# Optimization experiments

Measured on AMD Instinct MI355X. Metric: run time of the kernel, lower is better.

The kernel has to match this reference:

```python
import jax, jax.numpy as jnp
import numpy as np

N = 50000
E = 800000
IN_C = 128
HID_C = 64
OUT_C = 64
HEADS = 4
NEG_SLOPE = 0.2


def setup_inputs() -> dict:
    key = jax.random.key(0)
    ks = jax.random.split(key, 12)
    x = jax.random.normal(ks[0], (N, IN_C), dtype=jnp.float32)
    edge_index = jax.random.randint(ks[1], (2, E), 0, N, dtype=jnp.int32)
    s = 0.1
    # layer 1 params (GATConv: shared lin for src/dst, att vectors per head, bias over H*C)
    W1 = jax.random.normal(ks[2], (IN_C, HEADS * HID_C), dtype=jnp.float32) * s
    att_src1 = jax.random.normal(ks[3], (HEADS, HID_C), dtype=jnp.float32) * s
    att_dst1 = jax.random.normal(ks[4], (HEADS, HID_C), dtype=jnp.float32) * s
    b1 = jnp.zeros((HEADS * HID_C,), dtype=jnp.float32)
    # layer 2 params
    W2 = jax.random.normal(ks[5], (HEADS * HID_C, HEADS * OUT_C), dtype=jnp.float32) * s
    att_src2 = jax.random.normal(ks[6], (HEADS, OUT_C), dtype=jnp.float32) * s
    att_dst2 = jax.random.normal(ks[7], (HEADS, OUT_C), dtype=jnp.float32) * s
    b2 = jnp.zeros((HEADS * OUT_C,), dtype=jnp.float32)
    return {"x": x, "edge_index": edge_index,
            "W1": W1, "att_src1": att_src1, "att_dst1": att_dst1, "b1": b1,
            "W2": W2, "att_src2": att_src2, "att_dst2": att_dst2, "b2": b2}


def _segment_softmax(e, dst, n):
    # e: [E, H], softmax over edges sharing the same dst node, per head
    m = jax.ops.segment_max(e, dst, num_segments=n)        # [N, H]
    ex = jnp.exp(e - m[dst])
    z = jax.ops.segment_sum(ex, dst, num_segments=n)       # [N, H]
    return ex / (z[dst] + 1e-16)


def _gat_layer(x, src, dst, W, att_src, att_dst, bias, heads, out_c):
    n = x.shape[0]
    h = (x @ W).reshape(n, heads, out_c)                   # [N, H, C]
    a_s = jnp.einsum('nhc,hc->nh', h, att_src)             # [N, H]
    a_d = jnp.einsum('nhc,hc->nh', h, att_dst)
    e = jax.nn.leaky_relu(a_s[src] + a_d[dst], NEG_SLOPE)  # [E, H]
    alpha = _segment_softmax(e, dst, n)                    # [E, H]
    msg = alpha[:, :, None] * h[src]                       # [E, H, C]
    out = jax.ops.segment_sum(msg, dst, num_segments=n)    # [N, H, C]
    return out.reshape(n, heads * out_c) + bias


def reference(x, edge_index, W1, att_src1, att_dst1, b1, W2, att_src2, att_dst2, b2):
    # PyG GATConv adds self-loops by default
    loops = jnp.arange(N, dtype=edge_index.dtype)
    src = jnp.concatenate([edge_index[0], loops])
    dst = jnp.concatenate([edge_index[1], loops])
    h = jax.nn.elu(_gat_layer(x, src, dst, W1, att_src1, att_dst1, b1, HEADS, HID_C))
    out = jax.nn.elu(_gat_layer(h, src, dst, W2, att_src2, att_dst2, b2, HEADS, OUT_C))
    return out  # [N, HEADS*OUT_C]
```

## Files before the change

kernel.cpp:

```cpp
#include <hip/hip_runtime.h>
#include <hip/hip_fp16.h>
#include <math.h>


#define LEAKY_SLOPE 0.2f

typedef __attribute__((ext_vector_type(8))) short short8v;
typedef __attribute__((ext_vector_type(4))) float float4v;


__global__ void hist_kernel(const int* __restrict__ ei, int* __restrict__ cnt,
                            int E, int Etot) {
    int e = blockIdx.x * blockDim.x + threadIdx.x;
    if (e >= Etot) return;
    int dst = (e < E) ? ei[E + e] : (e - E);
    atomicAdd(&cnt[dst], 1);
}

__global__ __launch_bounds__(1024) void scan_block(const int* __restrict__ cnt,
                                                   int* __restrict__ row_start,
                                                   int* __restrict__ partials,
                                                   int n) {
    __shared__ int wsum[16];
    int tid = threadIdx.x, lane = tid & 63, wid = tid >> 6;
    int gi = blockIdx.x * 1024 + tid;
    int v = (gi < n) ? cnt[gi] : 0;
    int x = v;
#pragma unroll
    for (int off = 1; off < 64; off <<= 1) {
        int y = __shfl_up(x, off, 64);
        if (lane >= off) x += y;
    }
    if (lane == 63) wsum[wid] = x;
    __syncthreads();
    if (wid == 0 && lane < 16) {
        int w = wsum[lane];
#pragma unroll
        for (int off = 1; off < 16; off <<= 1) {
            int y = __shfl_up(w, off, 16);
            if (lane >= off) w += y;
        }
        wsum[lane] = w;
    }
    __syncthreads();
    int excl = x - v + ((wid > 0) ? wsum[wid - 1] : 0);
    if (gi < n) row_start[gi] = excl;
    if (tid == 1023) partials[blockIdx.x] = wsum[15];
}

__global__ void scan_partials(int* __restrict__ partials, int nb) {
    int lane = threadIdx.x;
    int v = (lane < nb) ? partials[lane] : 0;
    int x = v;
#pragma unroll
    for (int off = 1; off < 64; off <<= 1) {
        int y = __shfl_up(x, off, 64);
        if (lane >= off) x += y;
    }
    if (lane < nb) partials[lane] = x - v;
    if (lane == nb - 1) partials[nb] = x;
}

__global__ __launch_bounds__(1024) void scan_add(int* __restrict__ row_start,
                                                 const int* __restrict__ partials,
                                                 int n, int nb) {
    int gi = blockIdx.x * 1024 + threadIdx.x;
    if (gi < n) row_start[gi] += partials[blockIdx.x];
    if (gi == 0) row_start[n] = partials[nb];
}

__global__ void scatter_kernel(const int* __restrict__ ei,
                               const int* __restrict__ row_start,
                               int* __restrict__ fill,
                               int* __restrict__ edge_src, int E, int Etot) {
    int e = blockIdx.x * blockDim.x + threadIdx.x;
    if (e >= Etot) return;
    int src, dst;
    if (e < E) { src = ei[e]; dst = ei[E + e]; }
    else       { src = e - E; dst = e - E; }
    int pos = row_start[dst] + atomicAdd(&fill[dst], 1);
    edge_src[pos] = src;
}


__device__ __forceinline__ short bf16_rne(float f) {
    unsigned u = __float_as_uint(f);
    return (short)((u + 0x7FFFu + ((u >> 16) & 1u)) >> 16);
}

__device__ __forceinline__ void split_bf16(float f, short& hi, short& lo) {
    unsigned u = __float_as_uint(f);
    hi = (short)(u >> 16);
    float fhi = __uint_as_float(u & 0xFFFF0000u);
    float flo = f - fhi;
    lo = (short)(__float_as_uint(flo) >> 16);
}

template <int K>
__global__ __launch_bounds__(256) void gemm_mfma(
    const float* __restrict__ A, const float* __restrict__ B,
    __half* __restrict__ Ch, const float* __restrict__ att_src,
    const float* __restrict__ att_dst, float* __restrict__ a_s_out,
    float* __restrict__ a_d_out, int M) {
    __shared__ short As_hi[128][40];
    __shared__ short Bs_hi[128][40];
    __shared__ short Bs_lo[128][40];

    const int col0 = (blockIdx.x & 1) * 128;
    const int row0 = (blockIdx.x >> 1) * 128;
    const int tid = threadIdx.x;
    const int lane = tid & 63;
    const int wave = tid >> 6;
    const int wr = wave >> 1, wc = wave & 1;
    const int quad = lane >> 4, lc = lane & 15;

    float4v acc[4][4] = {};

    const int bn = tid & 127;
    const int bkh = (tid >> 7) * 16;

    for (int k0 = 0; k0 < K; k0 += 32) {
#pragma unroll
        for (int i = 0; i < 4; i++) {
            int slot = tid + i * 256;
            int r = slot >> 3;
            int kq = (slot & 7) * 4;
            float4 v = {0.f, 0.f, 0.f, 0.f};
            int gr = row0 + r;
            if (gr < M) v = *(const float4*)&A[(size_t)gr * K + k0 + kq];
            short4 h4;
            h4.x = bf16_rne(v.x); h4.y = bf16_rne(v.y);
            h4.z = bf16_rne(v.z); h4.w = bf16_rne(v.w);
            *(short4*)&As_hi[r][kq] = h4;
        }
        {
            float f[16];
#pragma unroll
            for (int j = 0; j < 16; j++)
                f[j] = B[(size_t)(k0 + bkh + j) * 256 + col0 + bn];
            short h8[16], l8[16];
#pragma unroll
            for (int j = 0; j < 16; j++) split_bf16(f[j], h8[j], l8[j]);
#pragma unroll
            for (int j = 0; j < 4; j++) {
                *(short4*)&Bs_hi[bn][bkh + j * 4] = *(short4*)&h8[j * 4];
                *(short4*)&Bs_lo[bn][bkh + j * 4] = *(short4*)&l8[j * 4];
            }
        }
        __syncthreads();

        short8v a_hi[4], b_hi[4], b_lo[4];
#pragma unroll
        for (int mt = 0; mt < 4; mt++) {
            int r = wr * 64 + mt * 16 + lc;
            a_hi[mt] = *(const short8v*)&As_hi[r][quad * 8];
        }
#pragma unroll
        for (int nt = 0; nt < 4; nt++) {
            int n = wc * 64 + nt * 16 + lc;
            b_hi[nt] = *(const short8v*)&Bs_hi[n][quad * 8];
            b_lo[nt] = *(const short8v*)&Bs_lo[n][quad * 8];
        }
#pragma unroll
        for (int mt = 0; mt < 4; mt++)
#pragma unroll
            for (int nt = 0; nt < 4; nt++) {
                acc[mt][nt] = __builtin_amdgcn_mfma_f32_16x16x32_bf16(
                    a_hi[mt], b_hi[nt], acc[mt][nt], 0, 0, 0);
                acc[mt][nt] = __builtin_amdgcn_mfma_f32_16x16x32_bf16(
                    a_hi[mt], b_lo[nt], acc[mt][nt], 0, 0, 0);
            }
        __syncthreads();
    }

    const int head = (col0 >> 6) + wc;
    float as_c[4], ad_c[4];
#pragma unroll
    for (int nt = 0; nt < 4; nt++) {
        as_c[nt] = att_src[head * 64 + nt * 16 + lc];
        ad_c[nt] = att_dst[head * 64 + nt * 16 + lc];
    }

#pragma unroll
    for (int mt = 0; mt < 4; mt++) {
#pragma unroll
        for (int r = 0; r < 4; r++) {
            int gr = row0 + wr * 64 + mt * 16 + quad * 4 + r;
            float ps = 0.f, pd = 0.f;
#pragma unroll
            for (int nt = 0; nt < 4; nt++) {
                float c = acc[mt][nt][r];
                ps = fmaf(c, as_c[nt], ps);
                pd = fmaf(c, ad_c[nt], pd);
                if (gr < M)
                    Ch[(size_t)gr * 256 + col0 + wc * 64 + nt * 16 + lc] =
                        __float2half(c);
            }
#pragma unroll
            for (int off = 1; off < 16; off <<= 1) {
                ps += __shfl_xor(ps, off, 64);
                pd += __shfl_xor(pd, off, 64);
            }
            if (lc == 0 && gr < M) {
                a_s_out[gr * 4 + head] = ps;
                a_d_out[gr * 4 + head] = pd;
            }
        }
    }
}


__global__ __launch_bounds__(256) void gat_aggregate(
    const __half* __restrict__ hh, const float* __restrict__ a_s,
    const float* __restrict__ a_d, const int* __restrict__ row_start,
    const int* __restrict__ edge_src, const float* __restrict__ bias,
    float* __restrict__ out, int n) {
    int wid = (blockIdx.x * blockDim.x + threadIdx.x) >> 6;
    int lane = threadIdx.x & 63;
    int half = lane >> 5, l32 = lane & 31;
    int node = wid * 2 + half;
    bool valid = (node < n);
    int nd = valid ? node : 0;
    int head = l32 >> 3;

    float ad = a_d[nd * 4 + head];
    int beg = row_start[nd];
    int end = valid ? row_start[nd + 1] : beg;

    float l = 0.f;
    float acc[8] = {};

    int s0 = 0, s1 = 0;
    float as0 = 0.f, as1 = 0.f;
    uint4 v0 = {0, 0, 0, 0}, v1 = {0, 0, 0, 0};
    if (beg < end) {
        s0 = edge_src[beg];
        as0 = a_s[s0 * 4 + head];
        v0 = *(const uint4*)&hh[(size_t)s0 * 256 + l32 * 8];
    }
    if (beg + 1 < end) {
        s1 = edge_src[beg + 1];
        as1 = a_s[s1 * 4 + head];
        v1 = *(const uint4*)&hh[(size_t)s1 * 256 + l32 * 8];
    }

    for (int i = beg; i < end; ++i) {
        int s2 = s1; float as2 = as1; uint4 v2 = v1;
        if (i + 2 < end) {
            s2 = edge_src[i + 2];
            as2 = a_s[s2 * 4 + head];
            v2 = *(const uint4*)&hh[(size_t)s2 * 256 + l32 * 8];
        }
        float e = as0 + ad;
        e = (e > 0.f) ? e : LEAKY_SLOPE * e;
        float w = __expf(e);
        l += w;
        const __half2* hp = (const __half2*)&v0;
#pragma unroll
        for (int j = 0; j < 4; j++) {
            float2 f = __half22float2(hp[j]);
            acc[2 * j]     = fmaf(w, f.x, acc[2 * j]);
            acc[2 * j + 1] = fmaf(w, f.y, acc[2 * j + 1]);
        }
        s0 = s1; as0 = as1; v0 = v1;
        s1 = s2; as1 = as2; v1 = v2;
    }

    if (valid) {
        float r = 1.f / l;
        float4 b0 = *(const float4*)&bias[l32 * 8];
        float4 b1 = *(const float4*)&bias[l32 * 8 + 4];
        float o[8];
        const float* bb = &b0.x;
        o[0] = fmaf(acc[0], r, b0.x); o[1] = fmaf(acc[1], r, b0.y);
        o[2] = fmaf(acc[2], r, b0.z); o[3] = fmaf(acc[3], r, b0.w);
        o[4] = fmaf(acc[4], r, b1.x); o[5] = fmaf(acc[5], r, b1.y);
        o[6] = fmaf(acc[6], r, b1.z); o[7] = fmaf(acc[7], r, b1.w);
        (void)bb;
#pragma unroll
        for (int j = 0; j < 8; j++)
            o[j] = (o[j] > 0.f) ? o[j] : __expf(o[j]) - 1.f;
        *(float4*)&out[(size_t)node * 256 + l32 * 8]     = *(float4*)&o[0];
        *(float4*)&out[(size_t)node * 256 + l32 * 8 + 4] = *(float4*)&o[4];
    }
}


extern "C" void kernel_launch(void* const* d_in, const int* in_sizes, int n_in,
                              void* d_out, int out_size, void* d_ws, size_t ws_size,
                              hipStream_t stream) {
    const float* x   = (const float*)d_in[0];
    const int*   ei  = (const int*)d_in[1];
    const float* W1  = (const float*)d_in[2];
    const float* as1 = (const float*)d_in[3];
    const float* ad1 = (const float*)d_in[4];
    const float* b1  = (const float*)d_in[5];
    const float* W2  = (const float*)d_in[6];
    const float* as2 = (const float*)d_in[7];
    const float* ad2 = (const float*)d_in[8];
    const float* b2  = (const float*)d_in[9];
    float* out = (float*)d_out;

    const int N = in_sizes[0] / 128;
    const int E = in_sizes[1] / 2;
    const int Etot = E + N;
    const int NB = (N + 1023) / 1024;

    __half* h_half = (__half*)d_ws;
    float* x1_buf  = (float*)(h_half + (size_t)N * 256);
    float* a_s     = x1_buf + (size_t)N * 256;
    float* a_d     = a_s + (size_t)N * 4;
    int*   cnt     = (int*)(a_d + (size_t)N * 4);
    int*   fill    = cnt + N;
    int*   row_st  = fill + N;
    int*   edge_src= row_st + (N + 1);
    int*   partials= edge_src + Etot;

    hipMemsetAsync(cnt, 0, sizeof(int) * 2 * (size_t)N, stream);
    int eblocks = (Etot + 255) / 256;
    hist_kernel<<<eblocks, 256, 0, stream>>>(ei, cnt, E, Etot);
    scan_block<<<NB, 1024, 0, stream>>>(cnt, row_st, partials, N);
    scan_partials<<<1, 64, 0, stream>>>(partials, NB);
    scan_add<<<NB, 1024, 0, stream>>>(row_st, partials, N, NB);
    scatter_kernel<<<eblocks, 256, 0, stream>>>(ei, row_st, fill, edge_src, E, Etot);

    dim3 ggrid(2 * ((N + 127) / 128));
    int ablocks = (N + 7) / 8;

    gemm_mfma<128><<<ggrid, 256, 0, stream>>>(x, W1, h_half, as1, ad1, a_s, a_d, N);
    gat_aggregate<<<ablocks, 256, 0, stream>>>(h_half, a_s, a_d, row_st, edge_src,
                                               b1, x1_buf, N);
    gemm_mfma<256><<<ggrid, 256, 0, stream>>>(x1_buf, W2, h_half, as2, ad2, a_s, a_d, N);
    gat_aggregate<<<ablocks, 256, 0, stream>>>(h_half, a_s, a_d, row_st, edge_src,
                                               b2, out, N);
}
```

Measured before the change: 409.6 us.

## Pack per-edge source and attention records, store layer-1 output as bf16

Adds a fill_rec kernel that packs each CSR edge's source index and its four fp16 source-attention logits into a 16-byte record. The aggregation loop can then fetch index and logit in one load and pipeline three feature gathers ahead. Layer-1 aggregation writes bf16 instead of fp32, and the second GEMM reads bf16 A directly, which halves that intermediate's traffic and drops a conversion. The costs are two extra edge-sized kernels, fp16 rounding of a_s, and bf16 storage of the hidden activations.

```diff
diff --git a/kernel.cpp b/kernel.cpp
--- a/kernel.cpp
+++ b/kernel.cpp
@@ -82,6 +82,17 @@
     edge_src[pos] = src;
 }
 
+__global__ void fill_rec(const int* __restrict__ edge_src,
+                         const __half* __restrict__ a_s_h,
+                         uint4* __restrict__ rec, int Etot) {
+    int i = blockIdx.x * blockDim.x + threadIdx.x;
+    if (i >= Etot) return;
+    int s = edge_src[i];
+    uint2 as8 = *(const uint2*)&a_s_h[(size_t)s * 4];
+    uint4 r = {(unsigned)s, as8.x, as8.y, 0u};
+    rec[i] = r;
+}
+
 
 __device__ __forceinline__ short bf16_rne(float f) {
     unsigned u = __float_as_uint(f);
@@ -96,11 +107,11 @@
     lo = (short)(__float_as_uint(flo) >> 16);
 }
 
-template <int K>
+template <int K, bool ABF16>
 __global__ __launch_bounds__(256) void gemm_mfma(
-    const float* __restrict__ A, const float* __restrict__ B,
+    const void* __restrict__ Ap, const float* __restrict__ B,
     __half* __restrict__ Ch, const float* __restrict__ att_src,
-    const float* __restrict__ att_dst, float* __restrict__ a_s_out,
+    const float* __restrict__ att_dst, __half* __restrict__ a_s_out,
     float* __restrict__ a_d_out, int M) {
     __shared__ short As_hi[128][40];
     __shared__ short Bs_hi[128][40];
@@ -120,18 +131,36 @@
     const int bkh = (tid >> 7) * 16;
 
     for (int k0 = 0; k0 < K; k0 += 32) {
-#pragma unroll
-        for (int i = 0; i < 4; i++) {
-            int slot = tid + i * 256;
-            int r = slot >> 3;
-            int kq = (slot & 7) * 4;
-            float4 v = {0.f, 0.f, 0.f, 0.f};
-            int gr = row0 + r;
-            if (gr < M) v = *(const float4*)&A[(size_t)gr * K + k0 + kq];
-            short4 h4;
-            h4.x = bf16_rne(v.x); h4.y = bf16_rne(v.y);
-            h4.z = bf16_rne(v.z); h4.w = bf16_rne(v.w);
-            *(short4*)&As_hi[r][kq] = h4;
+        if constexpr (ABF16) {
+            const short* Abf = (const short*)Ap;
+#pragma unroll
+            for (int i = 0; i < 2; i++) {
+                int slot = tid + i * 256;
+                int r = slot >> 2;
+                int ko = (slot & 3) * 8;
+                short8v v = {};
+                int gr = row0 + r;
+                if (gr < M) v = *(const short8v*)&Abf[(size_t)gr * K + k0 + ko];
+                short4 lo4 = {v[0], v[1], v[2], v[3]};
+                short4 hi4 = {v[4], v[5], v[6], v[7]};
+                *(short4*)&As_hi[r][ko] = lo4;
+                *(short4*)&As_hi[r][ko + 4] = hi4;
+            }
+        } else {
+            const float* A = (const float*)Ap;
+#pragma unroll
+            for (int i = 0; i < 4; i++) {
+                int slot = tid + i * 256;
+                int r = slot >> 3;
+                int kq = (slot & 7) * 4;
+                float4 v = {0.f, 0.f, 0.f, 0.f};
+                int gr = row0 + r;
+                if (gr < M) v = *(const float4*)&A[(size_t)gr * K + k0 + kq];
+                short4 h4;
+                h4.x = bf16_rne(v.x); h4.y = bf16_rne(v.y);
+                h4.z = bf16_rne(v.z); h4.w = bf16_rne(v.w);
+                *(short4*)&As_hi[r][kq] = h4;
+            }
         }
         {
             float f[16];
@@ -202,7 +231,7 @@
                 pd += __shfl_xor(pd, off, 64);
             }
             if (lc == 0 && gr < M) {
-                a_s_out[gr * 4 + head] = ps;
+                a_s_out[gr * 4 + head] = __float2half(ps);
                 a_d_out[gr * 4 + head] = pd;
             }
         }
@@ -210,11 +239,11 @@
 }
 
 
+template <bool OUT_BF16>
 __global__ __launch_bounds__(256) void gat_aggregate(
-    const __half* __restrict__ hh, const float* __restrict__ a_s,
+    const __half* __restrict__ hh, const uint4* __restrict__ rec,
     const float* __restrict__ a_d, const int* __restrict__ row_start,
-    const int* __restrict__ edge_src, const float* __restrict__ bias,
-    float* __restrict__ out, int n) {
+    const float* __restrict__ bias, void* __restrict__ outp, int n) {
     int wid = (blockIdx.x * blockDim.x + threadIdx.x) >> 6;
     int lane = threadIdx.x & 63;
     int half = lane >> 5, l32 = lane & 31;
@@ -230,58 +259,76 @@
     float l = 0.f;
     float acc[8] = {};
 
-    int s0 = 0, s1 = 0;
-    float as0 = 0.f, as1 = 0.f;
-    uint4 v0 = {0, 0, 0, 0}, v1 = {0, 0, 0, 0};
-    if (beg < end) {
-        s0 = edge_src[beg];
-        as0 = a_s[s0 * 4 + head];
-        v0 = *(const uint4*)&hh[(size_t)s0 * 256 + l32 * 8];
-    }
-    if (beg + 1 < end) {
-        s1 = edge_src[beg + 1];
-        as1 = a_s[s1 * 4 + head];
-        v1 = *(const uint4*)&hh[(size_t)s1 * 256 + l32 * 8];
-    }
-
-    for (int i = beg; i < end; ++i) {
-        int s2 = s1; float as2 = as1; uint4 v2 = v1;
-        if (i + 2 < end) {
-            s2 = edge_src[i + 2];
-            as2 = a_s[s2 * 4 + head];
-            v2 = *(const uint4*)&hh[(size_t)s2 * 256 + l32 * 8];
-        }
-        float e = as0 + ad;
-        e = (e > 0.f) ? e : LEAKY_SLOPE * e;
-        float w = __expf(e);
-        l += w;
-        const __half2* hp = (const __half2*)&v0;
-#pragma unroll
-        for (int j = 0; j < 4; j++) {
-            float2 f = __half22float2(hp[j]);
-            acc[2 * j]     = fmaf(w, f.x, acc[2 * j]);
-            acc[2 * j + 1] = fmaf(w, f.y, acc[2 * j + 1]);
-        }
-        s0 = s1; as0 = as1; v0 = v1;
-        s1 = s2; as1 = as2; v1 = v2;
-    }
+    int em1 = (end > beg) ? (end - 1) : beg;
+    uint4 r0 = rec[beg];
+    uint4 r1 = rec[min(beg + 1, em1)];
+    uint4 r2 = rec[min(beg + 2, em1)];
+
+#define GATH(rr) (*(const uint4*)&hh[(size_t)(rr).x * 256 + l32 * 8])
+#define PROC(rr, vv)                                                      \
+    {                                                                     \
+        unsigned u = (head & 2) ? (rr).z : (rr).y;                        \
+        unsigned short us = (head & 1) ? (unsigned short)(u >> 16)        \
+                                       : (unsigned short)(u & 0xFFFFu);   \
+        float as = __half2float(*(const __half*)&us);                     \
+        float e = as + ad;                                                \
+        e = (e > 0.f) ? e : LEAKY_SLOPE * e;                              \
+        float w = __expf(e);                                              \
+        l += w;                                                           \
+        const __half2* hp = (const __half2*)&(vv);                        \
+        _Pragma("unroll") for (int j = 0; j < 4; j++) {                   \
+            float2 f = __half22float2(hp[j]);                             \
+            acc[2 * j] = fmaf(w, f.x, acc[2 * j]);                        \
+            acc[2 * j + 1] = fmaf(w, f.y, acc[2 * j + 1]);                \
+        }                                                                 \
+    }
+
+    uint4 h0 = GATH(r0);
+    uint4 h1 = GATH(r1);
+    uint4 h2;
+
+    int s = beg;
+    while (s < end) {
+        h2 = GATH(r2);
+        PROC(r0, h0);
+        r0 = rec[min(s + 3, em1)];
+        if (++s >= end) break;
+        h0 = GATH(r0);
+        PROC(r1, h1);
+        r1 = rec[min(s + 3, em1)];
+        if (++s >= end) break;
+        h1 = GATH(r1);
+        PROC(r2, h2);
+        r2 = rec[min(s + 3, em1)];
+        ++s;
+    }
+#undef GATH
+#undef PROC
 
     if (valid) {
         float r = 1.f / l;
         float4 b0 = *(const float4*)&bias[l32 * 8];
         float4 b1 = *(const float4*)&bias[l32 * 8 + 4];
         float o[8];
-        const float* bb = &b0.x;
         o[0] = fmaf(acc[0], r, b0.x); o[1] = fmaf(acc[1], r, b0.y);
         o[2] = fmaf(acc[2], r, b0.z); o[3] = fmaf(acc[3], r, b0.w);
         o[4] = fmaf(acc[4], r, b1.x); o[5] = fmaf(acc[5], r, b1.y);
         o[6] = fmaf(acc[6], r, b1.z); o[7] = fmaf(acc[7], r, b1.w);
-        (void)bb;
 #pragma unroll
         for (int j = 0; j < 8; j++)
             o[j] = (o[j] > 0.f) ? o[j] : __expf(o[j]) - 1.f;
-        *(float4*)&out[(size_t)node * 256 + l32 * 8]     = *(float4*)&o[0];
-        *(float4*)&out[(size_t)node * 256 + l32 * 8 + 4] = *(float4*)&o[4];
+        if constexpr (OUT_BF16) {
+            short ob[8];
+#pragma unroll
+            for (int j = 0; j < 8; j++) ob[j] = bf16_rne(o[j]);
+            short* outb = (short*)outp;
+            *(short4*)&outb[(size_t)node * 256 + l32 * 8] = *(short4*)&ob[0];
+            *(short4*)&outb[(size_t)node * 256 + l32 * 8 + 4] = *(short4*)&ob[4];
+        } else {
+            float* outf = (float*)outp;
+            *(float4*)&outf[(size_t)node * 256 + l32 * 8] = *(float4*)&o[0];
+            *(float4*)&outf[(size_t)node * 256 + l32 * 8 + 4] = *(float4*)&o[4];
+        }
     }
 }
 
@@ -307,14 +354,15 @@
     const int NB = (N + 1023) / 1024;
 
     __half* h_half = (__half*)d_ws;
-    float* x1_buf  = (float*)(h_half + (size_t)N * 256);
-    float* a_s     = x1_buf + (size_t)N * 256;
-    float* a_d     = a_s + (size_t)N * 4;
-    int*   cnt     = (int*)(a_d + (size_t)N * 4);
-    int*   fill    = cnt + N;
-    int*   row_st  = fill + N;
-    int*   edge_src= row_st + (N + 1);
-    int*   partials= edge_src + Etot;
+    short*  x1_bf  = (short*)(h_half + (size_t)N * 256);
+    uint4*  rec    = (uint4*)(x1_bf + (size_t)N * 256);
+    __half* a_s_h  = (__half*)(rec + Etot);
+    float*  a_d    = (float*)(a_s_h + (size_t)N * 4);
+    int*    cnt    = (int*)(a_d + (size_t)N * 4);
+    int*    fill   = cnt + N;
+    int*    row_st = fill + N;
+    int*    edge_src = row_st + (N + 1);
+    int*    partials = edge_src + Etot;
 
     hipMemsetAsync(cnt, 0, sizeof(int) * 2 * (size_t)N, stream);
     int eblocks = (Etot + 255) / 256;
@@ -327,10 +375,14 @@
     dim3 ggrid(2 * ((N + 127) / 128));
     int ablocks = (N + 7) / 8;
 
-    gemm_mfma<128><<<ggrid, 256, 0, stream>>>(x, W1, h_half, as1, ad1, a_s, a_d, N);
-    gat_aggregate<<<ablocks, 256, 0, stream>>>(h_half, a_s, a_d, row_st, edge_src,
-                                               b1, x1_buf, N);
-    gemm_mfma<256><<<ggrid, 256, 0, stream>>>(x1_buf, W2, h_half, as2, ad2, a_s, a_d, N);
-    gat_aggregate<<<ablocks, 256, 0, stream>>>(h_half, a_s, a_d, row_st, edge_src,
-                                               b2, out, N);
-}
+    gemm_mfma<128, false><<<ggrid, 256, 0, stream>>>(x, W1, h_half, as1, ad1,
+                                                     a_s_h, a_d, N);
+    fill_rec<<<eblocks, 256, 0, stream>>>(edge_src, a_s_h, rec, Etot);
+    gat_aggregate<true><<<ablocks, 256, 0, stream>>>(h_half, rec, a_d, row_st,
+                                                     b1, x1_bf, N);
+    gemm_mfma<256, true><<<ggrid, 256, 0, stream>>>(x1_bf, W2, h_half, as2, ad2,
+                                                    a_s_h, a_d, N);
+    fill_rec<<<eblocks, 256, 0, stream>>>(edge_src, a_s_h, rec, Etot);
+    gat_aggregate<false><<<ablocks, 256, 0, stream>>>(h_half, rec, a_d, row_st,
+                                                      b2, out, N);
+}
```

Result: faster. 396.2 us (-3.3%).
